# Kernel optimization log

Measured on AMD Instinct MI355X. Metric: run time of the kernel, lower is better.

Reference implementation:

```python
import jax, jax.numpy as jnp
import numpy as np

N, D, V = 4096, 2048, 50257
IGNORE_INDEX = -100


def setup_inputs() -> dict:
    key = jax.random.key(0)
    k1, k2, k3 = jax.random.split(key, 3)
    x = jax.random.normal(k1, (N, D), dtype=jnp.float32)
    # lm_head.weight is [V, D]; the fused op receives weight.T -> [D, V]
    weight = jax.random.normal(k2, (D, V), dtype=jnp.float32) * (1.0 / np.sqrt(D))
    target = jax.random.randint(k3, (N,), 0, V, dtype=jnp.int64)
    return {"x": x, "weight": weight, "target": target}


def reference(x, weight, target):
    # Fused linear + cross-entropy (reduction='sum'), matching the Helion kernel math:
    # logits accumulated in fp32, online logsumexp == plain stable logsumexp.
    logits = jnp.matmul(x, weight, preferred_element_type=jnp.float32)  # [N, V] fp32
    lse = jax.nn.logsumexp(logits, axis=-1)                              # [N]
    tgt_idx = jnp.clip(target, 0, V - 1)                                 # safe gather
    target_logits = jnp.take_along_axis(logits, tgt_idx[:, None], axis=-1)[:, 0]
    per_token_loss = lse - target_logits                                 # [N]
    mask = (target != IGNORE_INDEX).astype(per_token_loss.dtype)
    ce_loss = jnp.sum(per_token_loss * mask)                             # reduction='sum'
    return ce_loss
```

## Files before the change

kernel.cpp:

```cpp
#include <hip/hip_runtime.h>
#include <hip/hip_bf16.h>
#include <stdint.h>

#define N_TOK 4096
#define DDIM  2048
#define VOCAB 50257
#define IGNORE_INDEX (-100)

#define BM 128
#define BN 128
#define BK 64
#define NT (DDIM / BK)
#define VCHUNKS ((VOCAB + BN - 1) / BN)
#define VP (VCHUNKS * BN)
#define ROW_TILES (N_TOK / BM)
#define GRID_MAIN (VCHUNKS * ROW_TILES)

#define W_SCALE 32.0f
#define W_INV   0.03125f
#define SCALE_1 0x7F7F7F7FU

typedef float f32x4  __attribute__((ext_vector_type(4)));
typedef float f32x16 __attribute__((ext_vector_type(16)));
typedef int   i32x4  __attribute__((ext_vector_type(4)));
typedef int   i32x8  __attribute__((ext_vector_type(8)));

__device__ __forceinline__ uint32_t pack2bf(float a, float b) {
  uint32_t ua = __float_as_uint(a);
  uint32_t ub = __float_as_uint(b);
  uint32_t ra = (ua + 0x7fffu + ((ua >> 16) & 1u)) >> 16;
  uint32_t rb = (ub + 0x7fffu + ((ub >> 16) & 1u)) & 0xffff0000u;
  return (ra & 0xffffu) | rb;
}

__device__ __forceinline__ uint32_t f32_to_e4m3(float f) {
  uint32_t u = __float_as_uint(f);
  uint32_t s = (u >> 24) & 0x80u;
  float a = fabsf(f);
  if (a >= 448.f) return s | 0x7Eu;
  if (a >= 0.015625f) {
    uint32_t m = __float_as_uint(a);
    m += 0x7FFFFu + ((m >> 20) & 1u);
    uint32_t e = (m >> 23) - 120u;
    return s | (e << 3) | ((m >> 20) & 7u);
  }
  uint32_t m = (uint32_t)rintf(a * 512.f);
  return s | m;
}

__device__ __forceinline__ void gload_lds16(const void* g, void* l) {
  __builtin_amdgcn_global_load_lds(
      (const __attribute__((address_space(1))) uint32_t*)g,
      (__attribute__((address_space(3))) uint32_t*)l, 16, 0, 0);
}


__global__ __launch_bounds__(256) void convert_x8(const float* __restrict__ x,
                                                  uint8_t* __restrict__ xp) {
  int t = blockIdx.x * 256 + threadIdx.x;
  const int n = t >> 7;
  const int q = t & 127;
  const float4* src = (const float4*)(x + (size_t)n * DDIM + q * 16);
  uint32_t u[4];
  #pragma unroll
  for (int g = 0; g < 4; ++g) {
    float4 f = src[g];
    u[g] = f32_to_e4m3(f.x) | (f32_to_e4m3(f.y) << 8) |
           (f32_to_e4m3(f.z) << 16) | (f32_to_e4m3(f.w) << 24);
  }
  const int T = q >> 2, rem = q & 3;
  const int hi = rem >> 1, p = rem & 1;
  const int tb = n >> 5, r5 = n & 31;
  const int l = hi * 32 + r5;
  uint8_t* dst = xp + (((size_t)tb * NT + T) * 2 + p) * 1024 + l * 16;
  *(uint4*)dst = make_uint4(u[0], u[1], u[2], u[3]);
}

__global__ __launch_bounds__(256) void transpose_w8(const float* __restrict__ w,
                                                    uint8_t* __restrict__ w8) {
  __shared__ float t[64][65];
  const int vb = blockIdx.x * 64;
  const int kb = blockIdx.y * 64;
  const int tid = threadIdx.x;
  const int tv = tid & 63, tk4 = tid >> 6;
  #pragma unroll
  for (int i = 0; i < 16; ++i) {
    int kl = tk4 + i * 4;
    int v = vb + tv;
    t[kl][tv] = (v < VOCAB) ? w[(size_t)(kb + kl) * VOCAB + v] * W_SCALE : 0.f;
  }
  __syncthreads();
  const int vl = tid >> 2, seg = tid & 3;
  uint32_t u[4];
  #pragma unroll
  for (int g = 0; g < 4; ++g) {
    u[g] = 0;
    #pragma unroll
    for (int j = 0; j < 4; ++j)
      u[g] |= f32_to_e4m3(t[seg * 16 + g * 4 + j][vl]) << (8 * j);
  }
  *(uint4*)(w8 + (size_t)(vb + vl) * DDIM + kb + seg * 16) =
      make_uint4(u[0], u[1], u[2], u[3]);
}

struct Bregs { i32x4 v[2][2]; };

__global__ __launch_bounds__(256, 3) void lmhead_main(
    const uint8_t* __restrict__ w8, const uint8_t* __restrict__ xp,
    const int* __restrict__ tgt,
    float2* __restrict__ partial, float* __restrict__ tlogit)
{
  __shared__ char lds[16384];
  __shared__ float2 stats[2][BM];

  const int bid = blockIdx.x;
  const int v = bid >> 5;
  const int r = bid & 31;
  const int v0 = v * BN;
  const int m0 = r * BM;
  const int tid = threadIdx.x;
  const int lane = tid & 63;
  const int wid = tid >> 6;
  const int wn = wid >> 1, wm = wid & 1;

  f32x16 acc[2][2];
  #pragma unroll
  for (int i = 0; i < 2; ++i)
    #pragma unroll
    for (int j = 0; j < 2; ++j) acc[i][j] = (f32x16)0.f;

  const int jj = lane >> 3;
  const int lu_s = (lane & 7) ^ jj;
  const int srow = 2 * jj + (lu_s >> 2);
  const int sk = (lu_s & 3) * 16;
  const uint8_t* wsrc = w8 + (size_t)(v0 + srow) * DDIM + sk;

  const int r5 = lane & 31, hi = lane >> 5;
  const int j7 = (r5 >> 1) & 7;
  const int lu0 = ((r5 & 1) << 2) | (hi << 1);
  const int rdoff = (r5 >> 1) * 128 + ((lu0 ^ j7) << 4);
  const int aoff0 = wn * 4096 + rdoff;

  const int tb0 = (m0 >> 5) + wm * 2;
  const uint8_t* xb0 = xp + ((size_t)tb0 * NT) * 2048 + lane * 16;
  const uint8_t* xb1 = xp + ((size_t)(tb0 + 1) * NT) * 2048 + lane * 16;

  auto stageA = [&](int T, int s) {
    char* Al = lds + s * 8192;
    const size_t ko = (size_t)T * BK;
    #pragma unroll
    for (int i = 0; i < 2; ++i) {
      int c = wid * 2 + i;
      gload_lds16(wsrc + (size_t)c * 16 * DDIM + ko, Al + c * 1024);
    }
  };
  auto loadB = [&](Bregs& B, int T) {
    const uint8_t* p0 = xb0 + (size_t)T * 2048;
    const uint8_t* p1 = xb1 + (size_t)T * 2048;
    B.v[0][0] = *(const i32x4*)(p0);
    B.v[0][1] = *(const i32x4*)(p0 + 1024);
    B.v[1][0] = *(const i32x4*)(p1);
    B.v[1][1] = *(const i32x4*)(p1 + 1024);
  };
  auto computeT = [&](const char* Al, const Bregs& B) {
    i32x8 bv[2];
    #pragma unroll
    for (int bj = 0; bj < 2; ++bj)
      bv[bj] = __builtin_shufflevector(B.v[bj][0], B.v[bj][1],
                                       0, 1, 2, 3, 4, 5, 6, 7);
    #pragma unroll
    for (int bi = 0; bi < 2; ++bi) {
      i32x4 a0 = *(const i32x4*)(Al + (aoff0 + bi * 2048));
      i32x4 a1 = *(const i32x4*)(Al + ((aoff0 ^ 16) + bi * 2048));
      i32x8 av = __builtin_shufflevector(a0, a1, 0, 1, 2, 3, 4, 5, 6, 7);
      #pragma unroll
      for (int bj = 0; bj < 2; ++bj)
        acc[bi][bj] = __builtin_amdgcn_mfma_scale_f32_32x32x64_f8f6f4(
            av, bv[bj], acc[bi][bj], 0 , 0 ,
            0, SCALE_1, 0, SCALE_1);
    }
  };

  Bregs B0, B1;
  stageA(0, 0);
  loadB(B0, 0);
  __syncthreads();

  for (int t = 0; t < NT; t += 2) {
    if (t + 1 < NT) { stageA(t + 1, 1); loadB(B1, t + 1); }
    computeT(lds, B0);
    __syncthreads();
    if (t + 2 < NT) { stageA(t + 2, 0); loadB(B0, t + 2); }
    computeT(lds + 8192, B1);
    __syncthreads();
  }

  #pragma unroll
  for (int bj = 0; bj < 2; ++bj) {
    const int m_g = m0 + wm * 64 + bj * 32 + r5;
    float vmax = -INFINITY;
    #pragma unroll
    for (int bi = 0; bi < 2; ++bi) {
      #pragma unroll
      for (int rg = 0; rg < 16; ++rg) {
        int n_g = v0 + wn * 64 + bi * 32 + (rg & 3) + 8 * (rg >> 2) + 4 * hi;
        if (n_g < VOCAB) vmax = fmaxf(vmax, acc[bi][bj][rg] * W_INV);
      }
    }
    vmax = fmaxf(vmax, __shfl_xor(vmax, 32, 64));
    float ssum = 0.f;
    const int t = tgt[m_g];
    #pragma unroll
    for (int bi = 0; bi < 2; ++bi) {
      #pragma unroll
      for (int rg = 0; rg < 16; ++rg) {
        int n_g = v0 + wn * 64 + bi * 32 + (rg & 3) + 8 * (rg >> 2) + 4 * hi;
        float val = acc[bi][bj][rg] * W_INV;
        if (n_g < VOCAB) ssum += __expf(val - vmax);
        if (n_g == t) tlogit[m_g] = val;
      }
    }
    ssum += __shfl_xor(ssum, 32, 64);
    if (hi == 0) stats[wn][wm * 64 + bj * 32 + r5] = make_float2(vmax, ssum);
  }
  __syncthreads();
  if (tid < BM) {
    float2 a = stats[0][tid], b = stats[1][tid];
    float M = fmaxf(a.x, b.x);
    float S = a.y * __expf(a.x - M) + b.y * __expf(b.x - M);
    partial[(size_t)(m0 + tid) * VCHUNKS + v] = make_float2(M, S);
  }
}

typedef short bf16x8 __attribute__((ext_vector_type(8)));

__global__ __launch_bounds__(256, 2) void lmhead_partial_fb(
    const float* __restrict__ x, const float* __restrict__ w,
    const int* __restrict__ tgt,
    float2* __restrict__ partial, float* __restrict__ tlogit)
{
  __shared__ uint4 xs[BM * 64 * 2 / 16];
  __shared__ uint4 wtl[BN * 64 * 2 / 16];
  __shared__ float2 stats[2][BM];

  const int bid = blockIdx.x;
  const int v = bid >> 5;
  const int r = bid & 31;
  const int v0 = v * BN;
  const int m0 = r * BM;
  const int tid = threadIdx.x;
  const int lane = tid & 63;
  const int wid = tid >> 6;
  const int wn = wid >> 1, wm = wid & 1;
  const int lr = lane & 15, lk = lane >> 4;

  f32x4 acc[4][4];
  #pragma unroll
  for (int i = 0; i < 4; ++i)
    #pragma unroll
    for (int j = 0; j < 4; ++j) acc[i][j] = (f32x4)0.f;

  char* xsb = (char*)xs;
  char* wtb = (char*)wtl;

  for (int kt = 0; kt < DDIM / 64; ++kt) {
    const int k0 = kt * 64;
    __syncthreads();
    #pragma unroll
    for (int i = 0; i < 4; ++i) {
      int t = tid + i * 256;
      int m = t >> 3, kg = t & 7;
      const float* gp = x + (size_t)(m0 + m) * DDIM + k0 + kg * 8;
      float4 f0 = *(const float4*)gp;
      float4 f1 = *(const float4*)(gp + 4);
      uint4 pk;
      pk.x = pack2bf(f0.x, f0.y); pk.y = pack2bf(f0.z, f0.w);
      pk.z = pack2bf(f1.x, f1.y); pk.w = pack2bf(f1.z, f1.w);
      int byte = (m * 128 + kg * 16) ^ ((m & 7) << 4);
      *(uint4*)(xsb + byte) = pk;
    }
    #pragma unroll
    for (int i = 0; i < 4; ++i) {
      int t = tid + i * 256;
      int n = t & 127, kg = t >> 7;
      int col = v0 + n;
      float f[8];
      if (col < VOCAB) {
        const float* gp = w + (size_t)(k0 + kg * 8) * VOCAB + col;
        #pragma unroll
        for (int kk = 0; kk < 8; ++kk) f[kk] = gp[(size_t)kk * VOCAB];
      } else {
        #pragma unroll
        for (int kk = 0; kk < 8; ++kk) f[kk] = 0.f;
      }
      uint4 pk;
      pk.x = pack2bf(f[0], f[1]); pk.y = pack2bf(f[2], f[3]);
      pk.z = pack2bf(f[4], f[5]); pk.w = pack2bf(f[6], f[7]);
      int byte = (n * 128 + kg * 16) ^ ((n & 7) << 4);
      *(uint4*)(wtb + byte) = pk;
    }
    __syncthreads();
    #pragma unroll
    for (int ks = 0; ks < 2; ++ks) {
      bf16x8 af[4], bfr[4];
      #pragma unroll
      for (int bi = 0; bi < 4; ++bi) {
        int row = wn * 64 + bi * 16 + lr;
        int byte = (row * 128 + ks * 64 + lk * 16) ^ ((row & 7) << 4);
        af[bi] = *(const bf16x8*)(wtb + byte);
      }
      #pragma unroll
      for (int bj = 0; bj < 4; ++bj) {
        int row = wm * 64 + bj * 16 + lr;
        int byte = (row * 128 + ks * 64 + lk * 16) ^ ((row & 7) << 4);
        bfr[bj] = *(const bf16x8*)(xsb + byte);
      }
      #pragma unroll
      for (int bi = 0; bi < 4; ++bi)
        #pragma unroll
        for (int bj = 0; bj < 4; ++bj)
          acc[bi][bj] = __builtin_amdgcn_mfma_f32_16x16x32_bf16(
              af[bi], bfr[bj], acc[bi][bj], 0, 0, 0);
    }
  }

  #pragma unroll
  for (int bj = 0; bj < 4; ++bj) {
    const int m_g = m0 + wm * 64 + bj * 16 + lr;
    float vmax = -INFINITY;
    #pragma unroll
    for (int bi = 0; bi < 4; ++bi)
      #pragma unroll
      for (int rg = 0; rg < 4; ++rg) {
        int n_g = v0 + wn * 64 + bi * 16 + lk * 4 + rg;
        if (n_g < VOCAB) vmax = fmaxf(vmax, acc[bi][bj][rg]);
      }
    vmax = fmaxf(vmax, __shfl_xor(vmax, 16, 64));
    vmax = fmaxf(vmax, __shfl_xor(vmax, 32, 64));
    float ssum = 0.f;
    const int t = tgt[m_g];
    #pragma unroll
    for (int bi = 0; bi < 4; ++bi)
      #pragma unroll
      for (int rg = 0; rg < 4; ++rg) {
        int n_g = v0 + wn * 64 + bi * 16 + lk * 4 + rg;
        float val = acc[bi][bj][rg];
        if (n_g < VOCAB) ssum += __expf(val - vmax);
        if (n_g == t) tlogit[m_g] = val;
      }
    ssum += __shfl_xor(ssum, 16, 64);
    ssum += __shfl_xor(ssum, 32, 64);
    if (lk == 0) stats[wn][wm * 64 + bj * 16 + lr] = make_float2(vmax, ssum);
  }
  __syncthreads();
  if (tid < BM) {
    float2 a = stats[0][tid], b = stats[1][tid];
    float M = fmaxf(a.x, b.x);
    float S = a.y * __expf(a.x - M) + b.y * __expf(b.x - M);
    partial[(size_t)(m0 + tid) * VCHUNKS + v] = make_float2(M, S);
  }
}

__device__ __forceinline__ void lse_merge(float& m, float& s, float M, float S) {
  if (S > 0.f) {
    if (M > m) { s = s * __expf(m - M) + S; m = M; }
    else       { s += S * __expf(M - m); }
  }
}

__global__ void lmhead_reduce(const float2* __restrict__ partial,
                              const float* __restrict__ tlogit,
                              const int* __restrict__ tgt,
                              float* __restrict__ out)
{
  const int wid = threadIdx.x >> 6;
  const int lane = threadIdx.x & 63;
  const int row = blockIdx.x * 4 + wid;
  float m = -INFINITY, s = 0.f;
  for (int c = lane; c < VCHUNKS; c += 64) {
    float2 p = partial[(size_t)row * VCHUNKS + c];
    lse_merge(m, s, p.x, p.y);
  }
  #pragma unroll
  for (int off = 1; off < 64; off <<= 1) {
    float M = __shfl_xor(m, off, 64);
    float S = __shfl_xor(s, off, 64);
    lse_merge(m, s, M, S);
  }
  if (lane == 0) {
    int t = tgt[row];
    if (t != IGNORE_INDEX) {
      float loss = m + __logf(s) - tlogit[row];
      atomicAdd(out, loss);
    }
  }
}

extern "C" void kernel_launch(void* const* d_in, const int* in_sizes, int n_in,
                              void* d_out, int out_size, void* d_ws, size_t ws_size,
                              hipStream_t stream) {
  const float* x = (const float*)d_in[0];
  const float* w = (const float*)d_in[1];
  const int* tgt = (const int*)d_in[2];
  float* out = (float*)d_out;

  const size_t w8_bytes = (size_t)VP * DDIM;
  const size_t x8_bytes = (size_t)N_TOK * DDIM;
  const size_t part_bytes = (size_t)N_TOK * VCHUNKS * 8;
  const size_t tl_bytes = (size_t)N_TOK * 4;
  const size_t need = w8_bytes + x8_bytes + part_bytes + tl_bytes;

  hipMemsetAsync(d_out, 0, sizeof(float), stream);

  if (ws_size >= need) {
    uint8_t* w8 = (uint8_t*)d_ws;
    uint8_t* xp = (uint8_t*)d_ws + w8_bytes;
    float2* partial = (float2*)((char*)d_ws + w8_bytes + x8_bytes);
    float* tlogit = (float*)((char*)d_ws + w8_bytes + x8_bytes + part_bytes);

    convert_x8<<<dim3(N_TOK * DDIM / 16 / 256), 256, 0, stream>>>(x, xp);
    transpose_w8<<<dim3(VP / 64, DDIM / 64), 256, 0, stream>>>(w, w8);
    lmhead_main<<<dim3(GRID_MAIN), 256, 0, stream>>>(w8, xp, tgt, partial, tlogit);
    lmhead_reduce<<<dim3(N_TOK / 4), 256, 0, stream>>>(partial, tlogit, tgt, out);
  } else {
    float2* partial = (float2*)d_ws;
    float* tlogit = (float*)((char*)d_ws + part_bytes);
    lmhead_partial_fb<<<dim3(GRID_MAIN), 256, 0, stream>>>(x, w, tgt, partial, tlogit);
    lmhead_reduce<<<dim3(N_TOK / 4), 256, 0, stream>>>(partial, tlogit, tgt, out);
  }
}
```

Before: 686.0 us.

## Deepen K-loop pipeline to prefetch two tiles ahead with partial vmcnt waits

Converts the double-buffered main loop into a deeper pipeline: four LDS stages for the weight tile and three register sets for the activation tile, issuing loads two iterations ahead. Full __syncthreads waits are replaced by s_waitcnt vmcnt with nonzero counts plus a raw barrier, so outstanding loads keep flowing during compute. This is meant to hide global memory latency better. It doubles LDS use and adds registers, which may reduce occupancy under launch_bounds(256,3), and the hand-counted vmcnt values must match the emitted loads to stay correct.

```diff
diff --git a/kernel.cpp b/kernel.cpp
--- a/kernel.cpp
+++ b/kernel.cpp
@@ -110,7 +110,7 @@
     const int* __restrict__ tgt,
     float2* __restrict__ partial, float* __restrict__ tlogit)
 {
-  __shared__ char lds[16384];
+  __shared__ char lds[32768];
   __shared__ float2 stats[2][BM];
 
   const int bid = blockIdx.x;
@@ -145,6 +145,8 @@
   const uint8_t* xb0 = xp + ((size_t)tb0 * NT) * 2048 + lane * 16;
   const uint8_t* xb1 = xp + ((size_t)(tb0 + 1) * NT) * 2048 + lane * 16;
 
+  Bregs B[3];
+
   auto stageA = [&](int T, int s) {
     char* Al = lds + s * 8192;
     const size_t ko = (size_t)T * BK;
@@ -154,19 +156,20 @@
       gload_lds16(wsrc + (size_t)c * 16 * DDIM + ko, Al + c * 1024);
     }
   };
-  auto loadB = [&](Bregs& B, int T) {
+  auto loadB = [&](int bs, int T) {
     const uint8_t* p0 = xb0 + (size_t)T * 2048;
     const uint8_t* p1 = xb1 + (size_t)T * 2048;
-    B.v[0][0] = *(const i32x4*)(p0);
-    B.v[0][1] = *(const i32x4*)(p0 + 1024);
-    B.v[1][0] = *(const i32x4*)(p1);
-    B.v[1][1] = *(const i32x4*)(p1 + 1024);
+    B[bs].v[0][0] = *(const i32x4*)(p0);
+    B[bs].v[0][1] = *(const i32x4*)(p0 + 1024);
+    B[bs].v[1][0] = *(const i32x4*)(p1);
+    B[bs].v[1][1] = *(const i32x4*)(p1 + 1024);
   };
-  auto computeT = [&](const char* Al, const Bregs& B) {
+  auto computeT = [&](int s, int bs) {
+    const char* Al = lds + s * 8192;
     i32x8 bv[2];
     #pragma unroll
     for (int bj = 0; bj < 2; ++bj)
-      bv[bj] = __builtin_shufflevector(B.v[bj][0], B.v[bj][1],
+      bv[bj] = __builtin_shufflevector(B[bs].v[bj][0], B[bs].v[bj][1],
                                        0, 1, 2, 3, 4, 5, 6, 7);
     #pragma unroll
     for (int bi = 0; bi < 2; ++bi) {
@@ -181,20 +184,28 @@
     }
   };
 
-  Bregs B0, B1;
-  stageA(0, 0);
-  loadB(B0, 0);
+  stageA(0, 0); loadB(0, 0);
+  stageA(1, 1); loadB(1, 1);
+  asm volatile("s_waitcnt vmcnt(10)" ::: "memory");
+  __builtin_amdgcn_s_barrier();
+  asm volatile("" ::: "memory");
+
+  #pragma unroll
+  for (int t = 0; t < NT; ++t) {
+    if (t + 2 < NT) { stageA(t + 2, (t + 2) & 3); loadB((t + 2) % 3, t + 2); }
+    computeT(t & 3, t % 3);
+    if (t < NT - 2) {
+      asm volatile("s_waitcnt vmcnt(10)" ::: "memory");
+    } else if (t == NT - 2) {
+      asm volatile("s_waitcnt vmcnt(4)" ::: "memory");
+    } else {
+      asm volatile("s_waitcnt vmcnt(0)" ::: "memory");
+    }
+    __builtin_amdgcn_s_barrier();
+    asm volatile("" ::: "memory");
+  }
+
   __syncthreads();
-
-  for (int t = 0; t < NT; t += 2) {
-    if (t + 1 < NT) { stageA(t + 1, 1); loadB(B1, t + 1); }
-    computeT(lds, B0);
-    __syncthreads();
-    if (t + 2 < NT) { stageA(t + 2, 0); loadB(B0, t + 2); }
-    computeT(lds + 8192, B1);
-    __syncthreads();
-  }
-
   #pragma unroll
   for (int bj = 0; bj < 2; ++bj) {
     const int m_g = m0 + wm * 64 + bj * 32 + r5;
```

Result: no change. 684.8 us (-0.2%).
